# Kernel optimization log

Hardware: AMD Instinct MI355X
Metric: run time of the kernel (lower is better)

Reference implementation:

```python
import jax, jax.numpy as jnp
import numpy as np

N = 50000
E = 800000
D_IN, D_HID, D_OUT = 256, 256, 128


def _xavier(key, shape):
    fan_in, fan_out = shape
    limit = float(np.sqrt(6.0 / (fan_in + fan_out)))
    return jax.random.uniform(key, shape, jnp.float32, -limit, limit)


def setup_inputs() -> dict:
    key = jax.random.key(0)
    ks = jax.random.split(key, 12)
    x = jax.random.normal(ks[0], (N, D_IN), jnp.float32)
    edge_index = jax.random.randint(ks[1], (2, E), 0, N, dtype=jnp.int64)
    batch = jnp.zeros((N,), jnp.int64)
    # per-layer: message weight W, linear weight LW (stored [in, out]), bias b
    w1 = _xavier(ks[2], (D_IN, D_HID))
    lw1 = _xavier(ks[3], (D_IN, D_HID))
    lb1 = jnp.zeros((D_HID,), jnp.float32)
    w2 = _xavier(ks[4], (D_HID, D_HID))
    lw2 = _xavier(ks[5], (D_HID, D_HID))
    lb2 = jnp.zeros((D_HID,), jnp.float32)
    w3 = _xavier(ks[6], (D_HID, D_OUT))
    lw3 = _xavier(ks[7], (D_HID, D_OUT))
    lb3 = jnp.zeros((D_OUT,), jnp.float32)
    return {"x": x, "edge_index": edge_index, "batch": batch,
            "w1": w1, "lw1": lw1, "lb1": lb1,
            "w2": w2, "lw2": lw2, "lb2": lb2,
            "w3": w3, "lw3": lw3, "lb3": lb3}


def _gcn_layer(x, W, LW, b, row, col, norm):
    # message: norm * (x_j @ W); equivalent and cheaper: transform nodes once, gather
    xw = x @ W                                   # [N, out]
    msg = norm[:, None] * xw[row]                # [E, out]
    agg = jax.ops.segment_sum(msg, col, num_segments=x.shape[0])  # scatter-add at col
    return agg + x @ LW + b                      # residual linear path


def reference(x, edge_index, batch, w1, lw1, lb1, w2, lw2, lb2, w3, lw3, lb3):
    row, col = edge_index[0], edge_index[1]
    ones = jnp.ones((row.shape[0],), x.dtype)
    out_deg = jax.ops.segment_sum(ones, row, num_segments=N)
    in_deg = jax.ops.segment_sum(ones, col, num_segments=N)
    # inf at zero-degree nodes never gets gathered (those nodes have no edges)
    norm = out_deg[row] ** -0.5 * in_deg[col] ** -0.5  # [E]

    h = jax.nn.relu(_gcn_layer(x, w1, lw1, lb1, row, col, norm))
    h = jax.nn.relu(_gcn_layer(h, w2, lw2, lb2, row, col, norm))
    h = jax.nn.sigmoid(_gcn_layer(h, w3, lw3, lb3, row, col, norm))
    return h
```

## Files before the change

### kernel.cpp

```cpp
#include <hip/hip_runtime.h>
#include <hip/hip_bf16.h>
#include <math.h>

#define NNODES 50000
#define NEDGES 800000
#define HNB 64
#define HCHUNK (NEDGES / HNB)
#define HBINS 50176
#define SCAN_NB 196

typedef short s8v __attribute__((ext_vector_type(8)));
typedef float f4v __attribute__((ext_vector_type(4)));
typedef unsigned char uchar8;
using bf16 = __hip_bfloat16;

static __device__ __forceinline__ float bflo(unsigned int x) {
    union { unsigned int i; float f; } c; c.i = x << 16; return c.f;
}
static __device__ __forceinline__ float bfhi(unsigned int x) {
    union { unsigned int i; float f; } c; c.i = x & 0xffff0000u; return c.f;
}

static __device__ __forceinline__ void gload16(const void* g, void* l) {
    __builtin_amdgcn_global_load_lds(
        (const __attribute__((address_space(1))) unsigned int*)g,
        (__attribute__((address_space(3))) unsigned int*)l, 16, 0, 0);
}


#define M1 (256 * 512)
#define M2 (256 * 512)
#define M3 (256 * 256)

__global__ __launch_bounds__(256) void k_packall(
        const float* __restrict__ w1, const float* __restrict__ lw1,
        const float* __restrict__ w2, const float* __restrict__ lw2,
        const float* __restrict__ w3, const float* __restrict__ lw3,
        bf16* __restrict__ o1, bf16* __restrict__ o2, bf16* __restrict__ o3) {
    int i = blockIdx.x * 256 + threadIdx.x;
    const float* W; const float* LW; bf16* O; int C; int j;
    if (i < M1)            { W = w1; LW = lw1; O = o1; C = 256; j = i; }
    else if (i < M1 + M2)  { W = w2; LW = lw2; O = o2; C = 256; j = i - M1; }
    else                   { W = w3; LW = lw3; O = o3; C = 128; j = i - M1 - M2; }
    int n = j >> 8, k = j & 255;
    float v = (n < C) ? W[k * C + n] : LW[k * C + (n - C)];
    O[j] = __float2bfloat16(v);
}


__global__ __launch_bounds__(256) void k_hist(const int* __restrict__ ei,
                                              uchar8* __restrict__ partials,
                                              uchar8* __restrict__ lrank) {
    __shared__ unsigned int h32[HBINS / 4];
    int b = blockIdx.x, row = blockIdx.y, t = threadIdx.x;
    for (int i = t; i < HBINS / 4; i += 256) h32[i] = 0;
    __syncthreads();
    int beg = b * HCHUNK, end = beg + HCHUNK;
    const int* p = ei + (size_t)row * NEDGES;
    if (row == 0) {
        for (int e = beg + t; e < end; e += 256) {
            int id = p[e];
            atomicAdd(&h32[id >> 2], 1u << (8 * (id & 3)));
        }
    } else {
        for (int e = beg + t; e < end; e += 256) {
            int id = p[e];
            unsigned int old = atomicAdd(&h32[id >> 2], 1u << (8 * (id & 3)));
            lrank[e] = (uchar8)((old >> (8 * (id & 3))) & 0xffu);
        }
    }
    __syncthreads();
    unsigned int* o32 = (unsigned int*)(partials + ((size_t)row * HNB + b) * HBINS);
    for (int i = t; i < HBINS / 4; i += 256) o32[i] = h32[i];
}

__global__ __launch_bounds__(256) void k_hist_reduce(uchar8* __restrict__ partials,
                                                     float* __restrict__ rsqrt_out,
                                                     int* __restrict__ in_cnt,
                                                     int* __restrict__ block_sums) {
    __shared__ int sm[256];
    int row = blockIdx.y;
    int i = blockIdx.x * 256 + threadIdx.x;
    if (row == 0) {
        const uchar8* p = partials + i;
        int s = 0;
#pragma unroll 4
        for (int b = 0; b < HNB; ++b) s += p[(size_t)b * HBINS];
        if (i < NNODES) rsqrt_out[i] = rsqrtf((float)s);
    } else {
        uchar8* p = partials + (size_t)HNB * HBINS + i;
        int run = 0;
        for (int b = 0; b < HNB; ++b) {
            int c = p[(size_t)b * HBINS];
            p[(size_t)b * HBINS] = (uchar8)run;
            run += c;
        }
        if (i < NNODES) in_cnt[i] = run;
        sm[threadIdx.x] = (i < NNODES) ? run : 0;
        __syncthreads();
        for (int off = 128; off > 0; off >>= 1) {
            if (threadIdx.x < off) sm[threadIdx.x] += sm[threadIdx.x + off];
            __syncthreads();
        }
        if (threadIdx.x == 0) block_sums[blockIdx.x] = sm[0];
    }
}


__global__ void k_scan_blocks(const int* __restrict__ block_sums, int* __restrict__ block_base, int nb) {
    __shared__ int s[256];
    int t = threadIdx.x;
    int v = (t < nb) ? block_sums[t] : 0;
    s[t] = v;
    __syncthreads();
    for (int off = 1; off < 256; off <<= 1) {
        int u = (t >= off) ? s[t - off] : 0;
        __syncthreads();
        s[t] += u;
        __syncthreads();
    }
    block_base[t] = s[t] - v;
}

__global__ void k_scan_final(const int* __restrict__ in_cnt, const int* __restrict__ block_base,
                             int* __restrict__ offsets) {
    __shared__ int s[256];
    int b = blockIdx.x, t = threadIdx.x;
    int i = b * 256 + t;
    int v = (i < NNODES) ? in_cnt[i] : 0;
    s[t] = v;
    __syncthreads();
    for (int off = 1; off < 256; off <<= 1) {
        int u = (t >= off) ? s[t - off] : 0;
        __syncthreads();
        s[t] += u;
        __syncthreads();
    }
    int excl = s[t] - v + block_base[b];
    if (i < NNODES) offsets[i] = excl;
    if (i == NNODES - 1) offsets[NNODES] = excl + v;
}

__global__ __launch_bounds__(256) void k_scatter_free(const int* __restrict__ ei,
                                                      const int* __restrict__ offsets,
                                                      const uchar8* __restrict__ partials,
                                                      const uchar8* __restrict__ lrank,
                                                      int* __restrict__ src_sorted) {
    int e = blockIdx.x * 256 + threadIdx.x;
    if (e < NEDGES) {
        int r = ei[e], c = ei[NEDGES + e];
        int b = e / HCHUNK;
        int pos = offsets[c] + (int)partials[(size_t)(HNB + b) * HBINS + c] + (int)lrank[e];
        src_sorted[pos] = r;
    }
}

template<int D, int ACT>
__global__ __launch_bounds__(64) void k_agg_fused(const bf16* __restrict__ xw,
                                                  const bf16* __restrict__ xlw,
                                                  const int* __restrict__ offsets,
                                                  const int* __restrict__ src_sorted,
                                                  const float* __restrict__ rsqrt_out,
                                                  const float* __restrict__ bias,
                                                  void* __restrict__ out) {
    const int L = D / 8;
    const int G = 64 / L;
    const int U = 4;
    int lane = threadIdx.x;
    int v = blockIdx.x;
    int g = lane / L, sl = lane % L;

    int beg = offsets[v], end = offsets[v + 1];
    int deg = end - beg;
    int dcap = min(deg, 64);

    int id = 0; float wl = 0.f;
    if (lane < dcap) {
        id = src_sorted[beg + lane];
        wl = rsqrt_out[id];
    }

    float acc[U][8];
#pragma unroll
    for (int u = 0; u < U; ++u)
#pragma unroll
        for (int c = 0; c < 8; ++c) acc[u][c] = 0.f;

    const ushort* base = (const ushort*)xw + sl * 8;

    for (int e0 = 0; e0 < dcap; e0 += G * U) {
#pragma unroll
        for (int u = 0; u < U; ++u) {
            int e = e0 + u * G + g;
            int s = __shfl(id, e & 63, 64);
            float w = __shfl(wl, e & 63, 64);
            if (e >= dcap) w = 0.f;
            uint4 q = *(const uint4*)(base + (size_t)s * D);
            acc[u][0] += w * bflo(q.x); acc[u][1] += w * bfhi(q.x);
            acc[u][2] += w * bflo(q.y); acc[u][3] += w * bfhi(q.y);
            acc[u][4] += w * bflo(q.z); acc[u][5] += w * bfhi(q.z);
            acc[u][6] += w * bflo(q.w); acc[u][7] += w * bfhi(q.w);
        }
    }
    for (int j = beg + 64 + g; j < end; j += G) {
        int s = src_sorted[j];
        float w = rsqrt_out[s];
        uint4 q = *(const uint4*)(base + (size_t)s * D);
        acc[0][0] += w * bflo(q.x); acc[0][1] += w * bfhi(q.x);
        acc[0][2] += w * bflo(q.y); acc[0][3] += w * bfhi(q.y);
        acc[0][4] += w * bflo(q.z); acc[0][5] += w * bfhi(q.z);
        acc[0][6] += w * bflo(q.w); acc[0][7] += w * bfhi(q.w);
    }

#pragma unroll
    for (int c = 0; c < 8; ++c) acc[0][c] = (acc[0][c] + acc[1][c]) + (acc[2][c] + acc[3][c]);
#pragma unroll
    for (int d = 32; d >= L; d >>= 1) {
#pragma unroll
        for (int c = 0; c < 8; ++c) acc[0][c] += __shfl_down(acc[0][c], d, 64);
    }

    if (lane < L) {
        float sc = (deg > 0) ? rsqrtf((float)deg) : 0.f;
        const ushort* lwp = (const ushort*)xlw + (size_t)v * D + sl * 8;
        uint4 ql = *(const uint4*)lwp;
        const float* bp = bias + sl * 8;
        float4 b0 = *(const float4*)bp, b1 = *(const float4*)(bp + 4);
        float h[8];
        h[0] = acc[0][0] * sc + bflo(ql.x) + b0.x;
        h[1] = acc[0][1] * sc + bfhi(ql.x) + b0.y;
        h[2] = acc[0][2] * sc + bflo(ql.y) + b0.z;
        h[3] = acc[0][3] * sc + bfhi(ql.y) + b0.w;
        h[4] = acc[0][4] * sc + bflo(ql.z) + b1.x;
        h[5] = acc[0][5] * sc + bfhi(ql.z) + b1.y;
        h[6] = acc[0][6] * sc + bflo(ql.w) + b1.z;
        h[7] = acc[0][7] * sc + bfhi(ql.w) + b1.w;
        if (ACT == 1) {
            union { bf16 hh[8]; uint4 u; } o;
#pragma unroll
            for (int c = 0; c < 8; ++c) o.hh[c] = __float2bfloat16(fmaxf(h[c], 0.f));
            *(uint4*)((ushort*)out + (size_t)v * D + sl * 8) = o.u;
        } else {
            float r[8];
#pragma unroll
            for (int c = 0; c < 8; ++c) r[c] = 1.f / (1.f + expf(-h[c]));
            float* op = (float*)out + (size_t)v * D + sl * 8;
            *(float4*)op = (float4){r[0], r[1], r[2], r[3]};
            *(float4*)(op + 4) = (float4){r[4], r[5], r[6], r[7]};
        }
    }
}

template<int C2, bool A_BF16>
__global__ __launch_bounds__(256) void k_gemm2(const void* __restrict__ Aptr,
                                               const bf16* __restrict__ BT,
                                               bf16* __restrict__ XW,
                                               bf16* __restrict__ XLW) {
    constexpr int R = NNODES;
    constexpr int DH = C2 / 2;
    constexpr int GX = (NNODES + 127) / 128;
    constexpr int GY = C2 / 128;
    constexpr int NWG = GX * GY;
    __shared__ bf16 As[128 * 32];
    __shared__ bf16 Bs[128 * 32];

    int o = blockIdx.x;
    constexpr int qq = NWG / 8, rr = NWG % 8;
    int xcd = o & 7, idx = o >> 3;
    int lt = (xcd < rr ? xcd * (qq + 1) : rr * (qq + 1) + (xcd - rr) * qq) + idx;
    int r0 = (lt / GY) * 128;
    int n0 = (lt % GY) * 128;

    int t = threadIdx.x;
    int wave = t >> 6, lane = t & 63;
    int wr = wave >> 1, wc = wave & 1;

    f4v acc[4][4];
#pragma unroll
    for (int mi = 0; mi < 4; ++mi)
#pragma unroll
        for (int ni = 0; ni < 4; ++ni) acc[mi][ni] = (f4v){0.f, 0.f, 0.f, 0.f};

    int sr = t >> 2;
    int sk = (t & 3) * 8;
    int fr = t >> 1, fs = (t & 1) * 16;

    for (int k0 = 0; k0 < 256; k0 += 32) {
        if (A_BF16) {
            const bf16* Ab = (const bf16*)Aptr;
            gload16(Ab + (size_t)min(r0 + sr, R - 1) * 256 + k0 + sk,
                    (char*)As + wave * 1024);
            gload16(Ab + (size_t)min(r0 + sr + 64, R - 1) * 256 + k0 + sk,
                    (char*)As + 4096 + wave * 1024);
        } else {
            const float* Af = (const float*)Aptr + (size_t)min(r0 + fr, R - 1) * 256 + k0 + fs;
            float4 f0 = ((const float4*)Af)[0];
            float4 f1 = ((const float4*)Af)[1];
            float4 f2 = ((const float4*)Af)[2];
            float4 f3 = ((const float4*)Af)[3];
            union { bf16 h[16]; uint4 u[2]; } cv;
            cv.h[0]  = __float2bfloat16(f0.x); cv.h[1]  = __float2bfloat16(f0.y);
            cv.h[2]  = __float2bfloat16(f0.z); cv.h[3]  = __float2bfloat16(f0.w);
            cv.h[4]  = __float2bfloat16(f1.x); cv.h[5]  = __float2bfloat16(f1.y);
            cv.h[6]  = __float2bfloat16(f1.z); cv.h[7]  = __float2bfloat16(f1.w);
            cv.h[8]  = __float2bfloat16(f2.x); cv.h[9]  = __float2bfloat16(f2.y);
            cv.h[10] = __float2bfloat16(f2.z); cv.h[11] = __float2bfloat16(f2.w);
            cv.h[12] = __float2bfloat16(f3.x); cv.h[13] = __float2bfloat16(f3.y);
            cv.h[14] = __float2bfloat16(f3.z); cv.h[15] = __float2bfloat16(f3.w);
            *(uint4*)&As[fr * 32 + fs]     = cv.u[0];
            *(uint4*)&As[fr * 32 + fs + 8] = cv.u[1];
        }
        gload16(BT + (size_t)(n0 + sr) * 256 + k0 + sk,
                (char*)Bs + wave * 1024);
        gload16(BT + (size_t)(n0 + sr + 64) * 256 + k0 + sk,
                (char*)Bs + 4096 + wave * 1024);
        __syncthreads();

        int lr = lane & 15, lk = (lane >> 4) * 8;
        s8v a[4], b[4];
#pragma unroll
        for (int mi = 0; mi < 4; ++mi)
            a[mi] = *(const s8v*)&As[(wr * 64 + mi * 16 + lr) * 32 + lk];
#pragma unroll
        for (int ni = 0; ni < 4; ++ni)
            b[ni] = *(const s8v*)&Bs[(wc * 64 + ni * 16 + lr) * 32 + lk];
#pragma unroll
        for (int mi = 0; mi < 4; ++mi)
#pragma unroll
            for (int ni = 0; ni < 4; ++ni)
                acc[mi][ni] = __builtin_amdgcn_mfma_f32_16x16x32_bf16(a[mi], b[ni], acc[mi][ni], 0, 0, 0);
        __syncthreads();
    }

    bool isXW = (n0 < DH);
    bf16* OutH = isXW ? XW : XLW;
    int   c0   = isXW ? n0 : n0 - DH;

    int lr = lane & 15, lq = (lane >> 4) * 4;
#pragma unroll
    for (int mi = 0; mi < 4; ++mi) {
#pragma unroll
        for (int rj = 0; rj < 4; ++rj) {
            int grow = r0 + wr * 64 + mi * 16 + lq + rj;
            if (grow < R) {
#pragma unroll
                for (int ni = 0; ni < 4; ++ni) {
                    OutH[(size_t)grow * DH + c0 + wc * 64 + ni * 16 + lr] =
                        __float2bfloat16(acc[mi][ni][rj]);
                }
            }
        }
    }
}


extern "C" void kernel_launch(void* const* d_in, const int* in_sizes, int n_in,
                              void* d_out, int out_size, void* d_ws, size_t ws_size,
                              hipStream_t stream) {
    const float* x   = (const float*)d_in[0];
    const int*   ei  = (const int*)d_in[1];
    const float* w1  = (const float*)d_in[3];
    const float* lw1 = (const float*)d_in[4];
    const float* lb1 = (const float*)d_in[5];
    const float* w2  = (const float*)d_in[6];
    const float* lw2 = (const float*)d_in[7];
    const float* lb2 = (const float*)d_in[8];
    const float* w3  = (const float*)d_in[9];
    const float* lw3 = (const float*)d_in[10];
    const float* lb3 = (const float*)d_in[11];
    float* out = (float*)d_out;

    char* ws = (char*)d_ws;
    size_t off = 0;
    auto alloc = [&](size_t bytes) -> void* {
        void* p = ws + off;
        off += (bytes + 255) & ~(size_t)255;
        return p;
    };
    int*    in_cnt     = (int*)alloc((size_t)HBINS * 4);
    float*  rsqrt_out  = (float*)alloc((size_t)HBINS * 4);
    int*    offsets    = (int*)alloc((size_t)(NNODES + 1) * 4);
    int*    block_sums = (int*)alloc((size_t)256 * 4);
    int*    block_base = (int*)alloc((size_t)256 * 4);
    uchar8* partials   = (uchar8*)alloc((size_t)2 * HNB * HBINS);
    uchar8* lrank      = (uchar8*)alloc((size_t)NEDGES);
    int*    src_sorted = (int*)alloc((size_t)NEDGES * 4);
    bf16*   wcat1      = (bf16*)alloc((size_t)256 * 512 * 2);
    bf16*   wcat2      = (bf16*)alloc((size_t)256 * 512 * 2);
    bf16*   wcat3      = (bf16*)alloc((size_t)256 * 256 * 2);
    bf16*   xw         = (bf16*)alloc((size_t)NNODES * 256 * 2);
    bf16*   xlw        = (bf16*)alloc((size_t)NNODES * 256 * 2);
    bf16*   h1         = (bf16*)alloc((size_t)NNODES * 256 * 2);
    bf16*   h2         = (bf16*)alloc((size_t)NNODES * 256 * 2);

    k_packall<<<(M1 + M2 + M3) / 256, 256, 0, stream>>>(
        w1, lw1, w2, lw2, w3, lw3, wcat1, wcat2, wcat3);

    k_hist<<<dim3(HNB, 2), 256, 0, stream>>>(ei, partials, lrank);
    k_hist_reduce<<<dim3(SCAN_NB, 2), 256, 0, stream>>>(partials, rsqrt_out, in_cnt, block_sums);
    k_scan_blocks<<<1, 256, 0, stream>>>(block_sums, block_base, SCAN_NB);
    k_scan_final<<<SCAN_NB, 256, 0, stream>>>(in_cnt, block_base, offsets);
    int eblocks = (NEDGES + 255) / 256;
    k_scatter_free<<<eblocks, 256, 0, stream>>>(ei, offsets, partials, lrank, src_sorted);

    k_gemm2<512, false><<<391 * 4, 256, 0, stream>>>(x, wcat1, xw, xlw);
    k_agg_fused<256, 1><<<NNODES, 64, 0, stream>>>(xw, xlw, offsets, src_sorted, rsqrt_out, lb1, h1);
    k_gemm2<512, true><<<391 * 4, 256, 0, stream>>>(h1, wcat2, xw, xlw);
    k_agg_fused<256, 1><<<NNODES, 64, 0, stream>>>(xw, xlw, offsets, src_sorted, rsqrt_out, lb2, h2);
    k_gemm2<256, true><<<391 * 2, 256, 0, stream>>>(h2, wcat3, xw, xlw);
    k_agg_fused<128, 2><<<NNODES, 64, 0, stream>>>(xw, xlw, offsets, src_sorted, rsqrt_out, lb3, out);
}
```

Before: 388.2 us.

## Make GEMM persistent with resident B tile, double-buffered swizzled A; merge scan kernels

The GEMM now runs as a persistent grid. Each workgroup loads its full 128x256 B column tile into LDS once, then loops over several 128-row strips, double-buffering A tiles with XOR-swizzled LDS layouts to avoid bank conflicts and overlap loads with MFMA. The separate block-scan kernel is removed: each final-scan block reduces the preceding block sums itself, saving one launch at the cost of redundant work. The larger LDS footprint (about 80KB) limits occupancy, and there are fewer workgroups than before.

```diff
diff --git a/kernel.cpp b/kernel.cpp
--- a/kernel.cpp
+++ b/kernel.cpp
@@ -107,25 +107,19 @@
 }
 
 
-__global__ void k_scan_blocks(const int* __restrict__ block_sums, int* __restrict__ block_base, int nb) {
-    __shared__ int s[256];
-    int t = threadIdx.x;
-    int v = (t < nb) ? block_sums[t] : 0;
-    s[t] = v;
-    __syncthreads();
-    for (int off = 1; off < 256; off <<= 1) {
-        int u = (t >= off) ? s[t - off] : 0;
-        __syncthreads();
-        s[t] += u;
-        __syncthreads();
-    }
-    block_base[t] = s[t] - v;
-}
-
-__global__ void k_scan_final(const int* __restrict__ in_cnt, const int* __restrict__ block_base,
+__global__ void k_scan_final(const int* __restrict__ in_cnt, const int* __restrict__ block_sums,
                              int* __restrict__ offsets) {
     __shared__ int s[256];
+    __shared__ int sb[256];
     int b = blockIdx.x, t = threadIdx.x;
+    sb[t] = (t < b) ? block_sums[t] : 0;
+    __syncthreads();
+    for (int off = 128; off > 0; off >>= 1) {
+        if (t < off) sb[t] += sb[t + off];
+        __syncthreads();
+    }
+    int base = sb[0];
+
     int i = b * 256 + t;
     int v = (i < NNODES) ? in_cnt[i] : 0;
     s[t] = v;
@@ -136,7 +130,7 @@
         s[t] += u;
         __syncthreads();
     }
-    int excl = s[t] - v + block_base[b];
+    int excl = s[t] - v + base;
     if (i < NNODES) offsets[i] = excl;
     if (i == NNODES - 1) offsets[NNODES] = excl + v;
 }
@@ -252,52 +246,67 @@
 }
 
 template<int C2, bool A_BF16>
-__global__ __launch_bounds__(256) void k_gemm2(const void* __restrict__ Aptr,
+__global__ __launch_bounds__(256) void k_gemm5(const void* __restrict__ Aptr,
                                                const bf16* __restrict__ BT,
                                                bf16* __restrict__ XW,
                                                bf16* __restrict__ XLW) {
     constexpr int R = NNODES;
     constexpr int DH = C2 / 2;
-    constexpr int GX = (NNODES + 127) / 128;
     constexpr int GY = C2 / 128;
-    constexpr int NWG = GX * GY;
-    __shared__ bf16 As[128 * 32];
-    __shared__ bf16 Bs[128 * 32];
-
-    int o = blockIdx.x;
-    constexpr int qq = NWG / 8, rr = NWG % 8;
-    int xcd = o & 7, idx = o >> 3;
-    int lt = (xcd < rr ? xcd * (qq + 1) : rr * (qq + 1) + (xcd - rr) * qq) + idx;
-    int r0 = (lt / GY) * 128;
-    int n0 = (lt % GY) * 128;
+    constexpr int NRT = 391;
+    constexpr int NB = (GY == 4) ? 131 : 196;
+    __shared__ bf16 Bs[128 * 256];
+    __shared__ bf16 As[2][128 * 32];
+
+    int bid = blockIdx.x;
+    int ct = bid % GY;
+    int strip = bid / GY;
+    int n0 = ct * 128;
 
     int t = threadIdx.x;
     int wave = t >> 6, lane = t & 63;
     int wr = wave >> 1, wc = wave & 1;
-
-    f4v acc[4][4];
-#pragma unroll
-    for (int mi = 0; mi < 4; ++mi)
-#pragma unroll
-        for (int ni = 0; ni < 4; ++ni) acc[mi][ni] = (f4v){0.f, 0.f, 0.f, 0.f};
-
-    int sr = t >> 2;
-    int sk = (t & 3) * 8;
-    int fr = t >> 1, fs = (t & 1) * 16;
-
-    for (int k0 = 0; k0 < 256; k0 += 32) {
+    int lr = lane & 15;
+    int kch = lane >> 4;
+
+    char* AsB0 = (char*)As[0];
+    char* AsB1 = (char*)As[1];
+    char* BsB  = (char*)Bs;
+
+    const bf16* Bsrc = BT + (size_t)n0 * 256;
+#pragma unroll
+    for (int i = 0; i < 16; ++i) {
+        int c  = i * 256 + t;
+        int cs = c ^ ((c >> 5) & 7);
+        gload16(Bsrc + (size_t)cs * 8, BsB + i * 4096 + wave * 1024);
+    }
+
+    int sr  = t >> 2;
+    int sks = (((t & 3) ^ (sr & 3))) * 8;
+    int fr  = t >> 1, fs = (t & 1) * 16;
+
+    const bf16*  Ab  = (const bf16*)Aptr;
+    const float* Af0 = (const float*)Aptr;
+
+    bool first = true;
+    for (int rt = strip; rt < NRT; rt += NB) {
+        int r0 = rt * 128;
+
+        f4v acc[4][4];
+#pragma unroll
+        for (int mi = 0; mi < 4; ++mi)
+#pragma unroll
+            for (int ni = 0; ni < 4; ++ni) acc[mi][ni] = (f4v){0.f, 0.f, 0.f, 0.f};
+
+        float4 f0, f1, f2, f3;
+
         if (A_BF16) {
-            const bf16* Ab = (const bf16*)Aptr;
-            gload16(Ab + (size_t)min(r0 + sr, R - 1) * 256 + k0 + sk,
-                    (char*)As + wave * 1024);
-            gload16(Ab + (size_t)min(r0 + sr + 64, R - 1) * 256 + k0 + sk,
-                    (char*)As + 4096 + wave * 1024);
+            gload16(Ab + (size_t)min(r0 + sr, R - 1) * 256 + sks, AsB0 + wave * 1024);
+            gload16(Ab + (size_t)min(r0 + sr + 64, R - 1) * 256 + sks, AsB0 + 4096 + wave * 1024);
         } else {
-            const float* Af = (const float*)Aptr + (size_t)min(r0 + fr, R - 1) * 256 + k0 + fs;
-            float4 f0 = ((const float4*)Af)[0];
-            float4 f1 = ((const float4*)Af)[1];
-            float4 f2 = ((const float4*)Af)[2];
-            float4 f3 = ((const float4*)Af)[3];
+            const float* Af = Af0 + (size_t)min(r0 + fr, R - 1) * 256 + fs;
+            f0 = ((const float4*)Af)[0]; f1 = ((const float4*)Af)[1];
+            f2 = ((const float4*)Af)[2]; f3 = ((const float4*)Af)[3];
             union { bf16 h[16]; uint4 u[2]; } cv;
             cv.h[0]  = __float2bfloat16(f0.x); cv.h[1]  = __float2bfloat16(f0.y);
             cv.h[2]  = __float2bfloat16(f0.z); cv.h[3]  = __float2bfloat16(f0.w);
@@ -307,50 +316,86 @@
             cv.h[10] = __float2bfloat16(f2.z); cv.h[11] = __float2bfloat16(f2.w);
             cv.h[12] = __float2bfloat16(f3.x); cv.h[13] = __float2bfloat16(f3.y);
             cv.h[14] = __float2bfloat16(f3.z); cv.h[15] = __float2bfloat16(f3.w);
-            *(uint4*)&As[fr * 32 + fs]     = cv.u[0];
-            *(uint4*)&As[fr * 32 + fs + 8] = cv.u[1];
-        }
-        gload16(BT + (size_t)(n0 + sr) * 256 + k0 + sk,
-                (char*)Bs + wave * 1024);
-        gload16(BT + (size_t)(n0 + sr + 64) * 256 + k0 + sk,
-                (char*)Bs + 4096 + wave * 1024);
+            int cb = (t & 1) * 2;
+            *(uint4*)(AsB0 + fr * 64 + (((cb + 0) ^ (fr & 3)) << 4)) = cv.u[0];
+            *(uint4*)(AsB0 + fr * 64 + (((cb + 1) ^ (fr & 3)) << 4)) = cv.u[1];
+        }
         __syncthreads();
-
-        int lr = lane & 15, lk = (lane >> 4) * 8;
-        s8v a[4], b[4];
-#pragma unroll
-        for (int mi = 0; mi < 4; ++mi)
-            a[mi] = *(const s8v*)&As[(wr * 64 + mi * 16 + lr) * 32 + lk];
-#pragma unroll
-        for (int ni = 0; ni < 4; ++ni)
-            b[ni] = *(const s8v*)&Bs[(wc * 64 + ni * 16 + lr) * 32 + lk];
-#pragma unroll
-        for (int mi = 0; mi < 4; ++mi)
-#pragma unroll
-            for (int ni = 0; ni < 4; ++ni)
-                acc[mi][ni] = __builtin_amdgcn_mfma_f32_16x16x32_bf16(a[mi], b[ni], acc[mi][ni], 0, 0, 0);
-        __syncthreads();
-    }
-
-    bool isXW = (n0 < DH);
-    bf16* OutH = isXW ? XW : XLW;
-    int   c0   = isXW ? n0 : n0 - DH;
-
-    int lr = lane & 15, lq = (lane >> 4) * 4;
-#pragma unroll
-    for (int mi = 0; mi < 4; ++mi) {
-#pragma unroll
-        for (int rj = 0; rj < 4; ++rj) {
-            int grow = r0 + wr * 64 + mi * 16 + lq + rj;
-            if (grow < R) {
-#pragma unroll
-                for (int ni = 0; ni < 4; ++ni) {
-                    OutH[(size_t)grow * DH + c0 + wc * 64 + ni * 16 + lr] =
-                        __float2bfloat16(acc[mi][ni][rj]);
+        first = false;
+
+        for (int kt = 0; kt < 8; ++kt) {
+            char* cur = (kt & 1) ? AsB1 : AsB0;
+            char* nxt = (kt & 1) ? AsB0 : AsB1;
+            int k1 = (kt + 1) * 32;
+            bool more = (kt < 7);
+
+            if (more) {
+                if (A_BF16) {
+                    gload16(Ab + (size_t)min(r0 + sr, R - 1) * 256 + k1 + sks, nxt + wave * 1024);
+                    gload16(Ab + (size_t)min(r0 + sr + 64, R - 1) * 256 + k1 + sks, nxt + 4096 + wave * 1024);
+                } else {
+                    const float* Af = Af0 + (size_t)min(r0 + fr, R - 1) * 256 + k1 + fs;
+                    f0 = ((const float4*)Af)[0]; f1 = ((const float4*)Af)[1];
+                    f2 = ((const float4*)Af)[2]; f3 = ((const float4*)Af)[3];
                 }
             }
-        }
-    }
+
+            s8v a[4], b[4];
+#pragma unroll
+            for (int mi = 0; mi < 4; ++mi) {
+                int row = wr * 64 + mi * 16 + lr;
+                a[mi] = *(const s8v*)(cur + row * 64 + ((kch ^ (row & 3)) << 4));
+            }
+            int ch = kt * 4 + kch;
+#pragma unroll
+            for (int ni = 0; ni < 4; ++ni) {
+                int row = wc * 64 + ni * 16 + lr;
+                b[ni] = *(const s8v*)(BsB + row * 512 + ((ch ^ (row & 7)) << 4));
+            }
+#pragma unroll
+            for (int mi = 0; mi < 4; ++mi)
+#pragma unroll
+                for (int ni = 0; ni < 4; ++ni)
+                    acc[mi][ni] = __builtin_amdgcn_mfma_f32_16x16x32_bf16(a[mi], b[ni], acc[mi][ni], 0, 0, 0);
+
+            if (more && !A_BF16) {
+                union { bf16 h[16]; uint4 u[2]; } cv;
+                cv.h[0]  = __float2bfloat16(f0.x); cv.h[1]  = __float2bfloat16(f0.y);
+                cv.h[2]  = __float2bfloat16(f0.z); cv.h[3]  = __float2bfloat16(f0.w);
+                cv.h[4]  = __float2bfloat16(f1.x); cv.h[5]  = __float2bfloat16(f1.y);
+                cv.h[6]  = __float2bfloat16(f1.z); cv.h[7]  = __float2bfloat16(f1.w);
+                cv.h[8]  = __float2bfloat16(f2.x); cv.h[9]  = __float2bfloat16(f2.y);
+                cv.h[10] = __float2bfloat16(f2.z); cv.h[11] = __float2bfloat16(f2.w);
+                cv.h[12] = __float2bfloat16(f3.x); cv.h[13] = __float2bfloat16(f3.y);
+                cv.h[14] = __float2bfloat16(f3.z); cv.h[15] = __float2bfloat16(f3.w);
+                int cb = (t & 1) * 2;
+                *(uint4*)(nxt + fr * 64 + (((cb + 0) ^ (fr & 3)) << 4)) = cv.u[0];
+                *(uint4*)(nxt + fr * 64 + (((cb + 1) ^ (fr & 3)) << 4)) = cv.u[1];
+            }
+            __syncthreads();
+        }
+
+        bool isXW = (n0 < DH);
+        bf16* OutH = isXW ? XW : XLW;
+        int   c0   = isXW ? n0 : n0 - DH;
+
+        int lq = (lane >> 4) * 4;
+#pragma unroll
+        for (int mi = 0; mi < 4; ++mi) {
+#pragma unroll
+            for (int rj = 0; rj < 4; ++rj) {
+                int grow = r0 + wr * 64 + mi * 16 + lq + rj;
+                if (grow < R) {
+#pragma unroll
+                    for (int ni = 0; ni < 4; ++ni) {
+                        OutH[(size_t)grow * DH + c0 + wc * 64 + ni * 16 + lr] =
+                            __float2bfloat16(acc[mi][ni][rj]);
+                    }
+                }
+            }
+        }
+    }
+    (void)first;
 }
 
 
@@ -381,7 +426,6 @@
     float*  rsqrt_out  = (float*)alloc((size_t)HBINS * 4);
     int*    offsets    = (int*)alloc((size_t)(NNODES + 1) * 4);
     int*    block_sums = (int*)alloc((size_t)256 * 4);
-    int*    block_base = (int*)alloc((size_t)256 * 4);
     uchar8* partials   = (uchar8*)alloc((size_t)2 * HNB * HBINS);
     uchar8* lrank      = (uchar8*)alloc((size_t)NEDGES);
     int*    src_sorted = (int*)alloc((size_t)NEDGES * 4);
@@ -398,15 +442,14 @@
 
     k_hist<<<dim3(HNB, 2), 256, 0, stream>>>(ei, partials, lrank);
     k_hist_reduce<<<dim3(SCAN_NB, 2), 256, 0, stream>>>(partials, rsqrt_out, in_cnt, block_sums);
-    k_scan_blocks<<<1, 256, 0, stream>>>(block_sums, block_base, SCAN_NB);
-    k_scan_final<<<SCAN_NB, 256, 0, stream>>>(in_cnt, block_base, offsets);
+    k_scan_final<<<SCAN_NB, 256, 0, stream>>>(in_cnt, block_sums, offsets);
     int eblocks = (NEDGES + 255) / 256;
     k_scatter_free<<<eblocks, 256, 0, stream>>>(ei, offsets, partials, lrank, src_sorted);
 
-    k_gemm2<512, false><<<391 * 4, 256, 0, stream>>>(x, wcat1, xw, xlw);
+    k_gemm5<512, false><<<4 * 131, 256, 0, stream>>>(x, wcat1, xw, xlw);
     k_agg_fused<256, 1><<<NNODES, 64, 0, stream>>>(xw, xlw, offsets, src_sorted, rsqrt_out, lb1, h1);
-    k_gemm2<512, true><<<391 * 4, 256, 0, stream>>>(h1, wcat2, xw, xlw);
+    k_gemm5<512, true><<<4 * 131, 256, 0, stream>>>(h1, wcat2, xw, xlw);
     k_agg_fused<256, 1><<<NNODES, 64, 0, stream>>>(xw, xlw, offsets, src_sorted, rsqrt_out, lb2, h2);
-    k_gemm2<256, true><<<391 * 2, 256, 0, stream>>>(h2, wcat3, xw, xlw);
+    k_gemm5<256, true><<<2 * 196, 256, 0, stream>>>(h2, wcat3, xw, xlw);
     k_agg_fused<128, 2><<<NNODES, 64, 0, stream>>>(xw, xlw, offsets, src_sorted, rsqrt_out, lb3, out);
 }
```

New measurement: 415.0 us. +6.9%, slower.

## Process eight nodes per wavefront in aggregation with prefetch of next neighbor list

Applied to the files above, without the earlier changes.

The aggregation kernel now assigns eight consecutive destination nodes to each 64-thread block instead of one. It loads all nine offsets at once and prefetches the next node's source ids and weights while the current node is being aggregated. The goal is to cut per-block launch and setup cost and to hide the latency of the dependent index loads. In exchange there are 8x fewer blocks, which lowers the number of waves available to hide gather latency, and work is serialized within each wave.

```diff
diff --git a/kernel.cpp b/kernel.cpp
--- a/kernel.cpp
+++ b/kernel.cpp
@@ -166,88 +166,111 @@
     const int L = D / 8;
     const int G = 64 / L;
     const int U = 4;
+    const int NPW = 8;
     int lane = threadIdx.x;
-    int v = blockIdx.x;
+    int v0 = blockIdx.x * NPW;
     int g = lane / L, sl = lane % L;
 
-    int beg = offsets[v], end = offsets[v + 1];
-    int deg = end - beg;
-    int dcap = min(deg, 64);
-
-    int id = 0; float wl = 0.f;
-    if (lane < dcap) {
-        id = src_sorted[beg + lane];
-        wl = rsqrt_out[id];
-    }
-
-    float acc[U][8];
-#pragma unroll
-    for (int u = 0; u < U; ++u)
-#pragma unroll
-        for (int c = 0; c < 8; ++c) acc[u][c] = 0.f;
+    int off_l = (lane <= NPW) ? offsets[v0 + lane] : 0;
+
+    int id_cur = 0; float wl_cur = 0.f;
+    {
+        int b0_ = __shfl(off_l, 0, 64);
+        int d0_ = min(__shfl(off_l, 1, 64) - b0_, 64);
+        if (lane < d0_) {
+            id_cur = src_sorted[b0_ + lane];
+            wl_cur = rsqrt_out[id_cur];
+        }
+    }
 
     const ushort* base = (const ushort*)xw + sl * 8;
 
-    for (int e0 = 0; e0 < dcap; e0 += G * U) {
-#pragma unroll
-        for (int u = 0; u < U; ++u) {
-            int e = e0 + u * G + g;
-            int s = __shfl(id, e & 63, 64);
-            float w = __shfl(wl, e & 63, 64);
-            if (e >= dcap) w = 0.f;
+    for (int i = 0; i < NPW; ++i) {
+        int v = v0 + i;
+        int beg = __shfl(off_l, i, 64);
+        int end = __shfl(off_l, i + 1, 64);
+        int deg = end - beg;
+        int dcap = min(deg, 64);
+
+        int id_nx = 0; float wl_nx = 0.f;
+        if (i + 1 < NPW) {
+            int bn = __shfl(off_l, i + 1, 64);
+            int dn = min(__shfl(off_l, i + 2, 64) - bn, 64);
+            if (lane < dn) {
+                id_nx = src_sorted[bn + lane];
+                wl_nx = rsqrt_out[id_nx];
+            }
+        }
+
+        float acc[U][8];
+#pragma unroll
+        for (int u = 0; u < U; ++u)
+#pragma unroll
+            for (int c = 0; c < 8; ++c) acc[u][c] = 0.f;
+
+        for (int e0 = 0; e0 < dcap; e0 += G * U) {
+#pragma unroll
+            for (int u = 0; u < U; ++u) {
+                int e = e0 + u * G + g;
+                int s = __shfl(id_cur, e & 63, 64);
+                float w = __shfl(wl_cur, e & 63, 64);
+                if (e >= dcap) w = 0.f;
+                uint4 q = *(const uint4*)(base + (size_t)s * D);
+                acc[u][0] += w * bflo(q.x); acc[u][1] += w * bfhi(q.x);
+                acc[u][2] += w * bflo(q.y); acc[u][3] += w * bfhi(q.y);
+                acc[u][4] += w * bflo(q.z); acc[u][5] += w * bfhi(q.z);
+                acc[u][6] += w * bflo(q.w); acc[u][7] += w * bfhi(q.w);
+            }
+        }
+        for (int j = beg + 64 + g; j < end; j += G) {
+            int s = src_sorted[j];
+            float w = rsqrt_out[s];
             uint4 q = *(const uint4*)(base + (size_t)s * D);
-            acc[u][0] += w * bflo(q.x); acc[u][1] += w * bfhi(q.x);
-            acc[u][2] += w * bflo(q.y); acc[u][3] += w * bfhi(q.y);
-            acc[u][4] += w * bflo(q.z); acc[u][5] += w * bfhi(q.z);
-            acc[u][6] += w * bflo(q.w); acc[u][7] += w * bfhi(q.w);
-        }
-    }
-    for (int j = beg + 64 + g; j < end; j += G) {
-        int s = src_sorted[j];
-        float w = rsqrt_out[s];
-        uint4 q = *(const uint4*)(base + (size_t)s * D);
-        acc[0][0] += w * bflo(q.x); acc[0][1] += w * bfhi(q.x);
-        acc[0][2] += w * bflo(q.y); acc[0][3] += w * bfhi(q.y);
-        acc[0][4] += w * bflo(q.z); acc[0][5] += w * bfhi(q.z);
-        acc[0][6] += w * bflo(q.w); acc[0][7] += w * bfhi(q.w);
-    }
-
-#pragma unroll
-    for (int c = 0; c < 8; ++c) acc[0][c] = (acc[0][c] + acc[1][c]) + (acc[2][c] + acc[3][c]);
-#pragma unroll
-    for (int d = 32; d >= L; d >>= 1) {
-#pragma unroll
-        for (int c = 0; c < 8; ++c) acc[0][c] += __shfl_down(acc[0][c], d, 64);
-    }
-
-    if (lane < L) {
-        float sc = (deg > 0) ? rsqrtf((float)deg) : 0.f;
-        const ushort* lwp = (const ushort*)xlw + (size_t)v * D + sl * 8;
-        uint4 ql = *(const uint4*)lwp;
-        const float* bp = bias + sl * 8;
-        float4 b0 = *(const float4*)bp, b1 = *(const float4*)(bp + 4);
-        float h[8];
-        h[0] = acc[0][0] * sc + bflo(ql.x) + b0.x;
-        h[1] = acc[0][1] * sc + bfhi(ql.x) + b0.y;
-        h[2] = acc[0][2] * sc + bflo(ql.y) + b0.z;
-        h[3] = acc[0][3] * sc + bfhi(ql.y) + b0.w;
-        h[4] = acc[0][4] * sc + bflo(ql.z) + b1.x;
-        h[5] = acc[0][5] * sc + bfhi(ql.z) + b1.y;
-        h[6] = acc[0][6] * sc + bflo(ql.w) + b1.z;
-        h[7] = acc[0][7] * sc + bfhi(ql.w) + b1.w;
-        if (ACT == 1) {
-            union { bf16 hh[8]; uint4 u; } o;
-#pragma unroll
-            for (int c = 0; c < 8; ++c) o.hh[c] = __float2bfloat16(fmaxf(h[c], 0.f));
-            *(uint4*)((ushort*)out + (size_t)v * D + sl * 8) = o.u;
-        } else {
-            float r[8];
-#pragma unroll
-            for (int c = 0; c < 8; ++c) r[c] = 1.f / (1.f + expf(-h[c]));
-            float* op = (float*)out + (size_t)v * D + sl * 8;
-            *(float4*)op = (float4){r[0], r[1], r[2], r[3]};
-            *(float4*)(op + 4) = (float4){r[4], r[5], r[6], r[7]};
-        }
+            acc[0][0] += w * bflo(q.x); acc[0][1] += w * bfhi(q.x);
+            acc[0][2] += w * bflo(q.y); acc[0][3] += w * bfhi(q.y);
+            acc[0][4] += w * bflo(q.z); acc[0][5] += w * bfhi(q.z);
+            acc[0][6] += w * bflo(q.w); acc[0][7] += w * bfhi(q.w);
+        }
+
+#pragma unroll
+        for (int c = 0; c < 8; ++c) acc[0][c] = (acc[0][c] + acc[1][c]) + (acc[2][c] + acc[3][c]);
+#pragma unroll
+        for (int d = 32; d >= L; d >>= 1) {
+#pragma unroll
+            for (int c = 0; c < 8; ++c) acc[0][c] += __shfl_down(acc[0][c], d, 64);
+        }
+
+        if (lane < L) {
+            float sc = (deg > 0) ? rsqrtf((float)deg) : 0.f;
+            const ushort* lwp = (const ushort*)xlw + (size_t)v * D + sl * 8;
+            uint4 ql = *(const uint4*)lwp;
+            const float* bp = bias + sl * 8;
+            float4 b0 = *(const float4*)bp, b1 = *(const float4*)(bp + 4);
+            float h[8];
+            h[0] = acc[0][0] * sc + bflo(ql.x) + b0.x;
+            h[1] = acc[0][1] * sc + bfhi(ql.x) + b0.y;
+            h[2] = acc[0][2] * sc + bflo(ql.y) + b0.z;
+            h[3] = acc[0][3] * sc + bfhi(ql.y) + b0.w;
+            h[4] = acc[0][4] * sc + bflo(ql.z) + b1.x;
+            h[5] = acc[0][5] * sc + bfhi(ql.z) + b1.y;
+            h[6] = acc[0][6] * sc + bflo(ql.w) + b1.z;
+            h[7] = acc[0][7] * sc + bfhi(ql.w) + b1.w;
+            if (ACT == 1) {
+                union { bf16 hh[8]; uint4 u; } o;
+#pragma unroll
+                for (int c = 0; c < 8; ++c) o.hh[c] = __float2bfloat16(fmaxf(h[c], 0.f));
+                *(uint4*)((ushort*)out + (size_t)v * D + sl * 8) = o.u;
+            } else {
+                float r[8];
+#pragma unroll
+                for (int c = 0; c < 8; ++c) r[c] = 1.f / (1.f + expf(-h[c]));
+                float* op = (float*)out + (size_t)v * D + sl * 8;
+                *(float4*)op = (float4){r[0], r[1], r[2], r[3]};
+                *(float4*)(op + 4) = (float4){r[4], r[5], r[6], r[7]};
+            }
+        }
+
+        id_cur = id_nx; wl_cur = wl_nx;
     }
 }
 
@@ -404,9 +427,9 @@
     k_scatter_free<<<eblocks, 256, 0, stream>>>(ei, offsets, partials, lrank, src_sorted);
 
     k_gemm2<512, false><<<391 * 4, 256, 0, stream>>>(x, wcat1, xw, xlw);
-    k_agg_fused<256, 1><<<NNODES, 64, 0, stream>>>(xw, xlw, offsets, src_sorted, rsqrt_out, lb1, h1);
+    k_agg_fused<256, 1><<<NNODES / 8, 64, 0, stream>>>(xw, xlw, offsets, src_sorted, rsqrt_out, lb1, h1);
     k_gemm2<512, true><<<391 * 4, 256, 0, stream>>>(h1, wcat2, xw, xlw);
-    k_agg_fused<256, 1><<<NNODES, 64, 0, stream>>>(xw, xlw, offsets, src_sorted, rsqrt_out, lb2, h2);
+    k_agg_fused<256, 1><<<NNODES / 8, 64, 0, stream>>>(xw, xlw, offsets, src_sorted, rsqrt_out, lb2, h2);
     k_gemm2<256, true><<<391 * 2, 256, 0, stream>>>(h2, wcat3, xw, xlw);
-    k_agg_fused<128, 2><<<NNODES, 64, 0, stream>>>(xw, xlw, offsets, src_sorted, rsqrt_out, lb3, out);
-}
+    k_agg_fused<128, 2><<<NNODES / 8, 64, 0, stream>>>(xw, xlw, offsets, src_sorted, rsqrt_out, lb3, out);
+}
```

Measured after the change: 425.1 us. 9.5% more time.
